# Kernel optimization log

Hardware: AMD Instinct MI355X
Metric: run time of the kernel (lower is better)

## Reference

```python
import jax, jax.numpy as jnp
import numpy as np

N_Q = 50000
BATCH = 512
SEQLEN = 500
MEM_SIZE = 64
DK = 128   # key_embedding_dim == key_memory_state_dim == final_fc_dim
DV = 256   # value_embedding_dim == value_memory_state_dim
FC = 128


def setup_inputs() -> dict:
    key = jax.random.key(0)
    ks = jax.random.split(key, 16)
    q_data = jax.random.randint(ks[0], (BATCH, SEQLEN), 0, N_Q + 1, dtype=jnp.int64)
    qa_data = jax.random.randint(ks[1], (BATCH, SEQLEN), 0, 2 * N_Q + 1, dtype=jnp.int64)
    u = jax.random.uniform(ks[2], (BATCH * SEQLEN, 1))
    target = jnp.where(u < 0.1, -1.0, jnp.round(jax.random.uniform(ks[3], (BATCH * SEQLEN, 1)))).astype(jnp.float32)
    # embedding tables with padding_idx=0 zeroed
    q_embed_W = (jax.random.normal(ks[4], (N_Q + 1, DK)) * (2.0 / DK) ** 0.5).at[0].set(0.0)
    qa_embed_W = (jax.random.normal(ks[5], (2 * N_Q + 1, DV)) * (2.0 / DV) ** 0.5).at[0].set(0.0)
    key_memory = jax.random.normal(ks[6], (MEM_SIZE, DK)) * (2.0 / DK) ** 0.5
    init_value_memory = jax.random.normal(ks[7], (MEM_SIZE, DV)) * (2.0 / DV) ** 0.5
    erase_W = jax.random.normal(ks[8], (DV, DV)) * (2.0 / DV) ** 0.5
    erase_b = jnp.zeros((DV,))
    add_W = jax.random.normal(ks[9], (DV, DV)) * (2.0 / DV) ** 0.5
    add_b = jnp.zeros((DV,))
    read_W = jax.random.normal(ks[10], (FC, DV + DK)) * (2.0 / (DV + DK)) ** 0.5
    read_b = jnp.zeros((FC,))
    pred_W = jax.random.normal(ks[11], (1, FC)) * (2.0 / FC) ** 0.5
    pred_b = jnp.zeros((1,))
    return dict(q_data=q_data, qa_data=qa_data, target=target,
                q_embed_W=q_embed_W, qa_embed_W=qa_embed_W,
                key_memory=key_memory, init_value_memory=init_value_memory,
                erase_W=erase_W, erase_b=erase_b, add_W=add_W, add_b=add_b,
                read_W=read_W, read_b=read_b, pred_W=pred_W, pred_b=pred_b)


def reference(q_data, qa_data, target, q_embed_W, qa_embed_W, key_memory,
              init_value_memory, erase_W, erase_b, add_W, add_b,
              read_W, read_b, pred_W, pred_b):
    B, S = q_data.shape
    q_e = q_embed_W[q_data]    # (B, S, DK)
    qa_e = qa_embed_W[qa_data]  # (B, S, DV)

    # Addressing weights do not depend on the value memory state -> batch them.
    cw = jax.nn.softmax(jnp.einsum('bsk,mk->bsm', q_e, key_memory), axis=-1)  # (B,S,M)
    erase = jax.nn.sigmoid(jnp.einsum('bsv,ev->bse', qa_e, erase_W) + erase_b)  # (B,S,DV)
    add = jnp.tanh(jnp.einsum('bsv,ev->bse', qa_e, add_W) + add_b)              # (B,S,DV)

    def step(mem, xs):
        w, er, ad = xs  # (B,M), (B,DV), (B,DV)
        read = jnp.einsum('bm,bmd->bd', w, mem)  # read before write
        mem = mem * (1.0 - w[:, :, None] * er[:, None, :]) + w[:, :, None] * ad[:, None, :]
        return mem, read

    init_mem = jnp.broadcast_to(init_value_memory, (B,) + init_value_memory.shape)
    _, reads = jax.lax.scan(step, init_mem,
                            (jnp.swapaxes(cw, 0, 1), jnp.swapaxes(erase, 0, 1), jnp.swapaxes(add, 0, 1)))
    reads = jnp.swapaxes(reads, 0, 1)  # (B, S, DV)

    predict_input = jnp.concatenate([reads, q_e], axis=-1).reshape(B * S, -1)
    h = jnp.tanh(predict_input @ read_W.T + read_b)
    logits = h @ pred_W.T + pred_b  # (B*S, 1)

    mask = target >= 0.0
    # numerically-stable BCE with logits
    bce = jnp.maximum(logits, 0.0) - logits * target + jnp.log1p(jnp.exp(-jnp.abs(logits)))
    denom = jnp.maximum(jnp.sum(mask.astype(logits.dtype)), 1.0)
    loss = jnp.sum(jnp.where(mask, bce, 0.0)) / denom
    # masked_select replaced by masked full-size outputs for static shapes
    pred_masked = jnp.where(mask, jax.nn.sigmoid(logits), 0.0)
    target_masked = jnp.where(mask, target, 0.0)
    return loss, pred_masked, target_masked
```

## Files before the change

### kernel.cpp

```cpp
#include <hip/hip_runtime.h>
#include <hip/hip_bf16.h>

#define BATCH 512
#define SEQ   500
#define BS    (BATCH*SEQ)
#define MEM   64
#define DK    128
#define DV    256
#define FC    128
#define KS    16

typedef float f32x4 __attribute__((ext_vector_type(4)));
typedef unsigned int u32x4 __attribute__((ext_vector_type(4)));
typedef unsigned int u32x2 __attribute__((ext_vector_type(2)));
typedef unsigned short u16x8 __attribute__((ext_vector_type(8)));
typedef __bf16 bf16x8 __attribute__((ext_vector_type(8)));

__device__ __forceinline__ float bf2f(unsigned short u){ return __uint_as_float(((unsigned)u)<<16); }
__device__ __forceinline__ unsigned short f2bfu(float x){
  unsigned u = __float_as_uint(x);
  return (unsigned short)((u + 0x7FFFu + ((u>>16)&1u)) >> 16);
}
__device__ __forceinline__ float sigf(float x){ return 1.f/(1.f+__expf(-x)); }
__device__ __forceinline__ float tanh_fast(float x){ return 2.f/(1.f+__expf(-2.f*x)) - 1.f; }

#define DPP_ADD(r, ctrl) { \
  int _s = __builtin_amdgcn_update_dpp(0, __builtin_bit_cast(int, r), ctrl, 0xF, 0xF, true); \
  r += __builtin_bit_cast(float, _s); \
}

__device__ __forceinline__ float ldF(const void* p, long i, int f32m){
  return f32m ? ((const float*)p)[i] : bf2f(((const unsigned short*)p)[i]);
}
__device__ __forceinline__ int ldI(const int* p, long i, int i64m){
  return i64m ? p[2*i] : p[i];
}
__device__ __forceinline__ void st8(unsigned short* dst, const void* src, long i, int f32m){
  if (f32m){
    const float* q = (const float*)src + i;
    f32x4 a = *(const f32x4*)q;
    f32x4 b = *(const f32x4*)(q+4);
    u16x8 o;
    o[0]=f2bfu(a[0]); o[1]=f2bfu(a[1]); o[2]=f2bfu(a[2]); o[3]=f2bfu(a[3]);
    o[4]=f2bfu(b[0]); o[5]=f2bfu(b[1]); o[6]=f2bfu(b[2]); o[7]=f2bfu(b[3]);
    *(u16x8*)dst = o;
  } else {
    *(u16x8*)dst = *(const u16x8*)((const unsigned short*)src + i);
  }
}
__device__ __forceinline__ void stOut(void* p, long i, float x, int f32m){
  if (f32m) ((float*)p)[i] = x;
  else ((unsigned short*)p)[i] = f2bfu(x);
}

__global__ void k_detect(const unsigned short* __restrict__ km, const int* __restrict__ qa,
                         int* __restrict__ flags, float* __restrict__ accum){
  int t = threadIdx.x;
  if (t < 2) accum[t] = 0.f;
  unsigned short u = km[2*t];
  int e = (u >> 7) & 0xFF;
  bool sane = (e==0) || (e>=100 && e<=140);
  unsigned long long sm = __ballot(sane);
  unsigned long long zm = __ballot(qa[2*t+1] == 0);
  if (t == 0){
    flags[0] = (__popcll(sm) < 48) ? 1 : 0;
    flags[1] = (zm == 0xFFFFFFFFFFFFFFFFull) ? 1 : 0;
  }
}

__global__ __launch_bounds__(256, 2) void k_cw(const int* __restrict__ qd,
    const void* __restrict__ qW, const void* __restrict__ keym,
    float* __restrict__ cw, const int* __restrict__ flags){
  const int f32m = flags[0], i64m = flags[1];
  __shared__ float keyT[DK][MEM];
  int t = threadIdx.x;
  for (int i=t;i<MEM*DK;i+=256){ int m=i&63, k=i>>6; keyT[k][m] = ldF(keym, (long)m*DK+k, f32m); }
  __syncthreads();
  long row = (long)blockIdx.x*256 + t;
  int qid = ldI(qd, row, i64m);
  long qb = (long)qid*DK;
  f32x4 A[16];
  #pragma unroll
  for (int g=0;g<16;g++) A[g] = (f32x4){0.f,0.f,0.f,0.f};
  for (int kk=0;kk<DK;kk+=8){
    float qv[8];
    if (f32m){
      const float* qp = (const float*)qW + qb + kk;
      f32x4 a=*(const f32x4*)qp, b=*(const f32x4*)(qp+4);
      qv[0]=a[0];qv[1]=a[1];qv[2]=a[2];qv[3]=a[3];qv[4]=b[0];qv[5]=b[1];qv[6]=b[2];qv[7]=b[3];
    } else {
      u16x8 u = *(const u16x8*)((const unsigned short*)qW + qb + kk);
      #pragma unroll
      for (int j=0;j<8;j++) qv[j]=bf2f(u[j]);
    }
    #pragma unroll
    for (int j=0;j<8;j++){
      float q = qv[j];
      #pragma unroll
      for (int g=0;g<16;g++){
        f32x4 kv = *(const f32x4*)&keyT[kk+j][g*4];
        f32x4 a = A[g];
        a[0]=fmaf(q,kv[0],a[0]); a[1]=fmaf(q,kv[1],a[1]);
        a[2]=fmaf(q,kv[2],a[2]); a[3]=fmaf(q,kv[3],a[3]);
        A[g]=a;
      }
    }
  }
  float mx = -1e30f;
  #pragma unroll
  for (int g=0;g<16;g++){
    f32x4 a = A[g];
    mx = fmaxf(mx, fmaxf(fmaxf(a[0],a[1]), fmaxf(a[2],a[3])));
  }
  float sum = 0.f;
  #pragma unroll
  for (int g=0;g<16;g++){
    f32x4 a = A[g];
    a[0]=__expf(a[0]-mx); a[1]=__expf(a[1]-mx); a[2]=__expf(a[2]-mx); a[3]=__expf(a[3]-mx);
    sum += (a[0]+a[1])+(a[2]+a[3]);
    A[g]=a;
  }
  float inv = 1.f/sum;
  float* outp = cw + row*MEM;
  #pragma unroll
  for (int g=0;g<16;g++){
    f32x4 a = A[g];
    f32x4 v = { a[0]*inv, a[1]*inv, a[2]*inv, a[3]*inv };
    *(f32x4*)(outp + g*4) = v;
  }
}

__global__ __launch_bounds__(256, 2) void k_ea(const int* __restrict__ qad, long row0,
    const void* __restrict__ qaW, const void* __restrict__ eW, const void* __restrict__ ebias,
    const void* __restrict__ aW, const void* __restrict__ abias,
    unsigned short* __restrict__ ea, const int* __restrict__ flags){
  const int f32m = flags[0], i64m = flags[1];
  __shared__ unsigned short As[128][40];
  __shared__ unsigned short Bs[128][40];
  __shared__ int rid[128];
  int t = threadIdx.x;
  int bm = blockIdx.x, bn = blockIdx.y;
  if (t<128) rid[t] = ldI(qad, row0 + (long)bm*128+t, i64m);
  int lane = t & 63, wid = t >> 6;
  int wr = wid >> 1, wc = wid & 1;
  f32x4 acc[4][4] = {};
  for (int k0=0;k0<DV;k0+=32){
    __syncthreads();
    #pragma unroll
    for (int j=0;j<2;j++){
      int c = t*2+j, r = c>>2, ko = (c&3)*8;
      st8(&As[r][ko], qaW, (long)rid[r]*DV + k0 + ko, f32m);
      int gn = bn*128 + r;
      if (gn < DV) st8(&Bs[r][ko], eW, (long)gn*DV + k0 + ko, f32m);
      else         st8(&Bs[r][ko], aW, (long)(gn-DV)*DV + k0 + ko, f32m);
    }
    __syncthreads();
    bf16x8 af[4], bfr[4];
    #pragma unroll
    for (int i=0;i<4;i++){
      af[i]  = __builtin_bit_cast(bf16x8, *(const u16x8*)&As[wr*64+i*16+(lane&15)][(lane>>4)*8]);
      bfr[i] = __builtin_bit_cast(bf16x8, *(const u16x8*)&Bs[wc*64+i*16+(lane&15)][(lane>>4)*8]);
    }
    #pragma unroll
    for (int i=0;i<4;i++)
      #pragma unroll
      for (int n=0;n<4;n++)
        acc[i][n] = __builtin_amdgcn_mfma_f32_16x16x32_bf16(af[i], bfr[n], acc[i][n],0,0,0);
  }
  #pragma unroll
  for (int i=0;i<4;i++)
    #pragma unroll
    for (int n=0;n<4;n++){
      int col = bn*128 + wc*64 + n*16 + (lane&15);
      float bias = (col<DV) ? ldF(ebias,col,f32m) : ldF(abias,col-DV,f32m);
      int dcol = (col<DV) ? 2*col : 2*(col-DV)+1;
      #pragma unroll
      for (int rix=0;rix<4;rix++){
        long rowg = (long)bm*128 + wr*64 + i*16 + (lane>>4)*4 + rix;
        float v = acc[i][n][rix] + bias;
        float o = (col<DV) ? sigf(v) : tanh_fast(v);
        ea[rowg*(2*DV) + dcol] = f2bfu(o);
      }
    }
}

#define SCAN_STEP2(srel) { \
  f32x4 W0 = *(const f32x4*)(wb + (srel)*MEM); \
  f32x4 W1 = *(const f32x4*)(wb + (srel)*MEM + 4); \
  u32x2 uu = *(const u32x2*)(eb + (srel)*256); \
  float er0 = __uint_as_float(uu[0] << 16); \
  float ad0 = __uint_as_float(uu[0] & 0xFFFF0000u); \
  float er1 = __uint_as_float(uu[1] << 16); \
  float ad1 = __uint_as_float(uu[1] & 0xFFFF0000u); \
  float ra0=0.f, ra1=0.f, rb0=0.f, rb1=0.f; \
  _Pragma("unroll") \
  for (int j=0; j<8; j++){ \
    float w = (j<4) ? W0[j] : W1[j-4]; \
    if (j & 1) ra1 = fmaf(w, MA[j], ra1); else ra0 = fmaf(w, MA[j], ra0); \
    float ta = fmaf(MA[j], er0, -ad0); \
    MA[j] = fmaf(-w, ta, MA[j]); \
    if (j & 1) rb1 = fmaf(w, MB[j], rb1); else rb0 = fmaf(w, MB[j], rb0); \
    float tb = fmaf(MB[j], er1, -ad1); \
    MB[j] = fmaf(-w, tb, MB[j]); \
  } \
  float r0 = ra0 + ra1; \
  float r1 = rb0 + rb1; \
  DPP_ADD(r0, 0x111); DPP_ADD(r0, 0x112); DPP_ADD(r0, 0x114); \
  DPP_ADD(r1, 0x111); DPP_ADD(r1, 0x112); DPP_ADD(r1, 0x114); \
  if (q == 7){ \
    unsigned pk; \
    asm("v_cvt_pk_bf16_f32 %0, %1, %2" : "=v"(pk) : "v"(r0), "v"(r1)); \
    rdu[(srel)*128] = pk; \
  } \
}

__global__ __launch_bounds__(1024, 4) void k_scan(const float* __restrict__ cw,
    const unsigned short* __restrict__ ea, const void* __restrict__ initm,
    unsigned short* __restrict__ rdout, const int* __restrict__ flags){
  const int f32m = flags[0];
  __shared__ float        w_lds[2][KS][MEM];
  __shared__ unsigned int ea_lds[2][KS][DV];
  int b = blockIdx.x;
  int t = threadIdx.x;
  int q = t & 7;
  int dp = t >> 3;
  int d0 = 2*dp;
  int m0 = q * 8;

  float MA[8], MB[8];
  #pragma unroll
  for (int g=0; g<8; g++){
    MA[g] = ldF(initm, (long)(m0+g)*DV + d0,   f32m);
    MB[g] = ldF(initm, (long)(m0+g)*DV + d0+1, f32m);
  }

  const float* cwb = cw + (long)b*SEQ*MEM;
  const unsigned int* epb = (const unsigned int*)(ea + (long)b*SEQ*(2*DV));
  unsigned int* rdu = (unsigned int*)(rdout + (long)b*SEQ*DV) + dp;

  {
    float wreg = cwb[t];
    u32x4 ereg = *(const u32x4*)(epb + t*4);
    ((float*)w_lds[0])[t] = wreg;
    *(u32x4*)((unsigned int*)ea_lds[0] + t*4) = ereg;
  }
  __syncthreads();

  int cur = 0;
  for (int st = 0; st < 31; st++){
    float wnext = cwb[(st+1)*KS*MEM + t];
    u32x4 enext = *(const u32x4*)(epb + (st+1)*KS*DV + t*4);

    const float* wb        = (const float*)w_lds[cur] + m0;
    const unsigned int* eb = (const unsigned int*)ea_lds[cur] + d0;
    #pragma unroll
    for (int srel=0; srel<KS; srel++){
      SCAN_STEP2(srel);
    }
    ((float*)w_lds[cur^1])[t] = wnext;
    *(u32x4*)((unsigned int*)ea_lds[cur^1] + t*4) = enext;
    rdu += KS*128;
    __syncthreads();
    cur ^= 1;
  }
  {
    const float* wb        = (const float*)w_lds[cur] + m0;
    const unsigned int* eb = (const unsigned int*)ea_lds[cur] + d0;
    #pragma unroll
    for (int srel=0; srel<4; srel++){
      SCAN_STEP2(srel);
    }
  }
}

__global__ __launch_bounds__(256, 2) void k_pred(const int* __restrict__ qd, long row0,
    const void* __restrict__ qW, const unsigned short* __restrict__ rds,
    const void* __restrict__ rW, const void* __restrict__ rb,
    const void* __restrict__ pW, const void* __restrict__ pb,
    const void* __restrict__ target,
    void* __restrict__ out, float* __restrict__ accum,
    const int* __restrict__ flags){
  const int f32m = flags[0], i64m = flags[1];
  __shared__ unsigned short As[128][40];
  __shared__ unsigned short Bs[128][40];
  __shared__ unsigned short hs[128][136];
  __shared__ int rid[128];
  int t = threadIdx.x;
  int bm = blockIdx.x;
  if (t<128) rid[t] = ldI(qd, row0 + (long)bm*128+t, i64m);
  int lane=t&63, wid=t>>6, wr=wid>>1, wc=wid&1;
  f32x4 acc[4][4] = {};
  for (int k0=0;k0<(DV+DK);k0+=32){
    __syncthreads();
    #pragma unroll
    for (int j=0;j<2;j++){
      int c=t*2+j, r=c>>2, ko=(c&3)*8;
      if (k0 < DV) st8(&As[r][ko], rds, ((long)bm*128+r)*DV + k0+ko, 0);
      else         st8(&As[r][ko], qW, (long)rid[r]*DK + (k0-DV)+ko, f32m);
      st8(&Bs[r][ko], rW, (long)r*(DV+DK) + k0+ko, f32m);
    }
    __syncthreads();
    bf16x8 af[4], bfr[4];
    #pragma unroll
    for (int i=0;i<4;i++){
      af[i]  = __builtin_bit_cast(bf16x8, *(const u16x8*)&As[wr*64+i*16+(lane&15)][(lane>>4)*8]);
      bfr[i] = __builtin_bit_cast(bf16x8, *(const u16x8*)&Bs[wc*64+i*16+(lane&15)][(lane>>4)*8]);
    }
    #pragma unroll
    for (int i=0;i<4;i++)
      #pragma unroll
      for (int n=0;n<4;n++)
        acc[i][n] = __builtin_amdgcn_mfma_f32_16x16x32_bf16(af[i], bfr[n], acc[i][n],0,0,0);
  }
  #pragma unroll
  for (int i=0;i<4;i++)
    #pragma unroll
    for (int n=0;n<4;n++){
      int col = wc*64 + n*16 + (lane&15);
      float bias = ldF(rb, col, f32m);
      #pragma unroll
      for (int rix=0;rix<4;rix++){
        int rowl = wr*64 + i*16 + (lane>>4)*4 + rix;
        hs[rowl][col] = f2bfu(tanh_fast(acc[i][n][rix] + bias));
      }
    }
  __syncthreads();
  float bces = 0.f, cnts = 0.f;
  if (t < 128){
    float lg = ldF(pb, 0, f32m);
    #pragma unroll
    for (int cc=0;cc<FC;cc++) lg = fmaf(bf2f(hs[t][cc]), ldF(pW, cc, f32m), lg);
    long rowg = row0 + (long)bm*128 + t;
    float tg = ldF(target, rowg, f32m);
    bool mask = tg >= 0.f;
    float e = __expf(-fabsf(lg));
    float bce = fmaxf(lg, 0.f) - lg*tg + __logf(1.f + e);
    bces = mask ? bce : 0.f;
    cnts = mask ? 1.f : 0.f;
    stOut(out, 1 + rowg, mask ? sigf(lg) : 0.f, f32m);
    stOut(out, 1 + BS + rowg, mask ? tg : 0.f, f32m);
  }
  #pragma unroll
  for (int off=32; off>0; off>>=1){ bces += __shfl_down(bces, off); cnts += __shfl_down(cnts, off); }
  if ((t & 63) == 0 && t < 128){
    atomicAdd(&accum[0], bces);
    atomicAdd(&accum[1], cnts);
  }
}

__global__ void k_loss(const float* __restrict__ accum, void* __restrict__ out,
                       const int* __restrict__ flags){
  if (threadIdx.x == 0){
    float denom = fmaxf(accum[1], 1.f);
    stOut(out, 0, accum[0]/denom, flags[0]);
  }
}

extern "C" void kernel_launch(void* const* d_in, const int* in_sizes, int n_in,
                              void* d_out, int out_size, void* d_ws, size_t ws_size,
                              hipStream_t stream) {
  const int* q_data  = (const int*)d_in[0];
  const int* qa_data = (const int*)d_in[1];
  const void* target = d_in[2];
  const void* qW   = d_in[3];
  const void* qaW  = d_in[4];
  const void* keym = d_in[5];
  const void* initm= d_in[6];
  const void* eW   = d_in[7];
  const void* eb   = d_in[8];
  const void* aW   = d_in[9];
  const void* ab   = d_in[10];
  const void* rW   = d_in[11];
  const void* rb   = d_in[12];
  const void* pW   = d_in[13];
  const void* pb   = d_in[14];

  char* ws = (char*)d_ws;
  const size_t CW_OFF = 256;
  const size_t CW_BYTES = (size_t)BS*MEM*4;
  const size_t EA_OFF = CW_OFF + CW_BYTES;
  float* accum = (float*)ws;
  int* flags = (int*)(ws + 64);
  float* cw = (float*)(ws + CW_OFF);

  const long per_batch = (long)SEQ*(2*DV)*2 + (long)SEQ*DV*2;
  long rem = (long)ws_size - (long)EA_OFF;
  int bchunk = 512;
  while (bchunk > 32 && per_batch*bchunk > rem) bchunk >>= 1;

  const size_t EA_BYTES = (size_t)bchunk*SEQ*(2*DV)*2;
  unsigned short* ea = (unsigned short*)(ws + EA_OFF);
  unsigned short* rd = (unsigned short*)(ws + EA_OFF + EA_BYTES);

  k_detect<<<1, 64, 0, stream>>>((const unsigned short*)keym, qa_data, flags, accum);
  k_cw  <<<BS/256, 256, 0, stream>>>(q_data, qW, keym, cw, flags);

  int nchunk = BATCH / bchunk;
  for (int c = 0; c < nchunk; c++){
    long b0 = (long)c * bchunk;
    int rows = bchunk * SEQ;
    k_ea  <<<dim3(rows/128, 4), 256, 0, stream>>>(qa_data, b0*SEQ, qaW, eW, eb, aW, ab, ea, flags);
    k_scan<<<bchunk, 1024, 0, stream>>>(cw + b0*SEQ*MEM, ea, initm, rd, flags);
    k_pred<<<rows/128, 256, 0, stream>>>(q_data, b0*SEQ, qW, rd, rW, rb, pW, pb,
                                         target, d_out, accum, flags);
  }
  k_loss<<<1, 64, 0, stream>>>(accum, d_out, flags);
}
```

Baseline: 1.058 ms.

## Retile erase/add GEMM so each block covers all 512 output columns

The erase/add projection kernel now gives each block 64 gathered rows and all 512 output columns (erase plus add), replacing the earlier 128x128 tiles spread over a 4-wide grid dimension. Each embedding row is gathered from the large qa table once instead of four times, which cuts random-gather traffic. In exchange, every block reloads the full 512x32 weight slice per k-step, shared memory grows to about 46 KB, and per-thread accumulators double to 32 MFMA tiles. The higher register and LDS pressure may reduce occupancy under the 2-blocks-per-SM launch bound.

```diff
diff --git a/kernel.cpp b/kernel.cpp
--- a/kernel.cpp
+++ b/kernel.cpp
@@ -135,53 +135,60 @@
     const void* __restrict__ aW, const void* __restrict__ abias,
     unsigned short* __restrict__ ea, const int* __restrict__ flags){
   const int f32m = flags[0], i64m = flags[1];
-  __shared__ unsigned short As[128][40];
-  __shared__ unsigned short Bs[128][40];
-  __shared__ int rid[128];
+  __shared__ unsigned short As[64][40];
+  __shared__ unsigned short Bs[512][40];
+  __shared__ int rid[64];
   int t = threadIdx.x;
-  int bm = blockIdx.x, bn = blockIdx.y;
-  if (t<128) rid[t] = ldI(qad, row0 + (long)bm*128+t, i64m);
+  int bm = blockIdx.x;
+  if (t < 64) rid[t] = ldI(qad, row0 + (long)bm*64 + t, i64m);
   int lane = t & 63, wid = t >> 6;
-  int wr = wid >> 1, wc = wid & 1;
-  f32x4 acc[4][4] = {};
+  f32x4 acc[4][8] = {};
   for (int k0=0;k0<DV;k0+=32){
     __syncthreads();
-    #pragma unroll
-    for (int j=0;j<2;j++){
-      int c = t*2+j, r = c>>2, ko = (c&3)*8;
+    {
+      int r = t >> 2, ko = (t & 3)*8;
       st8(&As[r][ko], qaW, (long)rid[r]*DV + k0 + ko, f32m);
-      int gn = bn*128 + r;
-      if (gn < DV) st8(&Bs[r][ko], eW, (long)gn*DV + k0 + ko, f32m);
-      else         st8(&Bs[r][ko], aW, (long)(gn-DV)*DV + k0 + ko, f32m);
+    }
+    #pragma unroll
+    for (int j=0;j<4;j++){
+      int idx = t + j*256; int r = idx>>2, ko = (idx&3)*8;
+      st8(&Bs[r][ko], eW, (long)r*DV + k0 + ko, f32m);
+    }
+    #pragma unroll
+    for (int j=4;j<8;j++){
+      int idx = t + j*256; int r = idx>>2, ko = (idx&3)*8;
+      st8(&Bs[r][ko], aW, (long)(r-DV)*DV + k0 + ko, f32m);
     }
     __syncthreads();
-    bf16x8 af[4], bfr[4];
+    bf16x8 af[4], bfr[8];
+    #pragma unroll
+    for (int i=0;i<4;i++)
+      af[i] = __builtin_bit_cast(bf16x8, *(const u16x8*)&As[i*16+(lane&15)][(lane>>4)*8]);
+    #pragma unroll
+    for (int n=0;n<8;n++)
+      bfr[n] = __builtin_bit_cast(bf16x8, *(const u16x8*)&Bs[wid*128+n*16+(lane&15)][(lane>>4)*8]);
+    #pragma unroll
+    for (int i=0;i<4;i++)
+      #pragma unroll
+      for (int n=0;n<8;n++)
+        acc[i][n] = __builtin_amdgcn_mfma_f32_16x16x32_bf16(af[i], bfr[n], acc[i][n],0,0,0);
+  }
+  #pragma unroll
+  for (int n=0;n<8;n++){
+    int col = wid*128 + n*16 + (lane&15);
+    float bias = (col<DV) ? ldF(ebias,col,f32m) : ldF(abias,col-DV,f32m);
+    int dcol = (col<DV) ? 2*col : 2*(col-DV)+1;
     #pragma unroll
     for (int i=0;i<4;i++){
-      af[i]  = __builtin_bit_cast(bf16x8, *(const u16x8*)&As[wr*64+i*16+(lane&15)][(lane>>4)*8]);
-      bfr[i] = __builtin_bit_cast(bf16x8, *(const u16x8*)&Bs[wc*64+i*16+(lane&15)][(lane>>4)*8]);
-    }
-    #pragma unroll
-    for (int i=0;i<4;i++)
-      #pragma unroll
-      for (int n=0;n<4;n++)
-        acc[i][n] = __builtin_amdgcn_mfma_f32_16x16x32_bf16(af[i], bfr[n], acc[i][n],0,0,0);
-  }
-  #pragma unroll
-  for (int i=0;i<4;i++)
-    #pragma unroll
-    for (int n=0;n<4;n++){
-      int col = bn*128 + wc*64 + n*16 + (lane&15);
-      float bias = (col<DV) ? ldF(ebias,col,f32m) : ldF(abias,col-DV,f32m);
-      int dcol = (col<DV) ? 2*col : 2*(col-DV)+1;
       #pragma unroll
       for (int rix=0;rix<4;rix++){
-        long rowg = (long)bm*128 + wr*64 + i*16 + (lane>>4)*4 + rix;
+        long rowg = (long)bm*64 + i*16 + (lane>>4)*4 + rix;
         float v = acc[i][n][rix] + bias;
         float o = (col<DV) ? sigf(v) : tanh_fast(v);
         ea[rowg*(2*DV) + dcol] = f2bfu(o);
       }
     }
+  }
 }
 
 #define SCAN_STEP2(srel) { \
@@ -399,7 +406,7 @@
   for (int c = 0; c < nchunk; c++){
     long b0 = (long)c * bchunk;
     int rows = bchunk * SEQ;
-    k_ea  <<<dim3(rows/128, 4), 256, 0, stream>>>(qa_data, b0*SEQ, qaW, eW, eb, aW, ab, ea, flags);
+    k_ea  <<<rows/64, 256, 0, stream>>>(qa_data, b0*SEQ, qaW, eW, eb, aW, ab, ea, flags);
     k_scan<<<bchunk, 1024, 0, stream>>>(cw + b0*SEQ*MEM, ea, initm, rd, flags);
     k_pred<<<rows/128, 256, 0, stream>>>(q_data, b0*SEQ, qW, rd, rW, rb, pW, pb,
                                          target, d_out, accum, flags);
```

Result: slower. 1.187 ms (+12.1%).
